# Optimization experiments

Hardware: AMD Instinct MI355X
Metric: run time of the kernel (lower is better)

## Reference

```python
import jax, jax.numpy as jnp
import numpy as np

B, T, N, DIN, HID, ED, K = 64, 12, 1024, 2, 64, 10, 2

def setup_inputs() -> dict:
    key = jax.random.key(0)
    ks = jax.random.split(key, 18)
    g = lambda i, shape, s=0.1: jax.random.normal(ks[i], shape, jnp.float32) * s
    return dict(
        x=g(0, (B, T, N, DIN), 1.0),
        node_embeddings=g(1, (N, ED), 1.0),
        # GCRN cell 0 (dim_in=DIN): gate -> 2*HID, update -> HID
        Wg0=g(2, (ED, K, DIN + HID, 2 * HID)), bg0=g(3, (ED, 2 * HID)),
        Wu0=g(4, (ED, K, DIN + HID, HID)),     bu0=g(5, (ED, HID)),
        # GCRN cell 1 (dim_in=HID)
        Wg1=g(6, (ED, K, 2 * HID, 2 * HID)),   bg1=g(7, (ED, 2 * HID)),
        Wu1=g(8, (ED, K, 2 * HID, HID)),       bu1=g(9, (ED, HID)),
        # RelatinoShipConv: pointwise Linear(input_dim -> rnn_units), torch [out,in]
        Wr=g(10, (HID, DIN)), br=g(11, (HID,)),
        # end_conv1: Linear(HID,HID, bias=False) (num_layers>1 branch)
        W1=g(12, (HID, HID)),
        # self.conv: Conv2d(horizon, horizon, (1, HID+1), bias=False), OIHW
        Wc=g(13, (T, T, 1, HID + 1)),
        # end_conv2: Conv2d(horizon, horizon, (1, HID), bias)
        W2=g(14, (T, T, 1, HID)), b2=g(15, (T,)),
        # end_conv3: Conv2d(horizon, horizon, (1, 2), dilation (1, HID), bias)
        W3=g(16, (T, T, 1, 2)), b3=g(17, (T,)),
    )

def _avwgcn(x, supports, E, Wp, bp):
    # x:[B,N,C], supports:[K,N,N], E:[N,ED] -> [B,N,O]  (AGCRN adaptive graph conv)
    xg = jnp.einsum('knm,bmc->bnkc', supports, x)
    W = jnp.einsum('ne,ekio->nkio', E, Wp)
    b = E @ bp
    return jnp.einsum('bnki,nkio->bno', xg, W) + b

def _cell(xt, h, supports, E, Wg, bg, Wu, bu):
    # GCRN GRU cell
    zr = jax.nn.sigmoid(_avwgcn(jnp.concatenate([xt, h], -1), supports, E, Wg, bg))
    z, r = jnp.split(zr, 2, -1)
    hc = jnp.tanh(_avwgcn(jnp.concatenate([xt, z * h], -1), supports, E, Wu, bu))
    return r * h + (1.0 - r) * hc

def _conv2d(x, w, b=None, rhs_dilation=(1, 1)):
    y = jax.lax.conv_general_dilated(x, w, (1, 1), 'VALID',
        rhs_dilation=rhs_dilation, dimension_numbers=('NCHW', 'OIHW', 'NCHW'))
    return y if b is None else y + b[None, :, None, None]

def _forward(x, E, Wg0, bg0, Wu0, bu0, Wg1, bg1, Wu1, bu1, Wr, br, W1, Wc, W2, b2, W3, b3):
    A = jax.nn.softmax(jax.nn.relu(E @ E.T), axis=1)
    supports = jnp.stack([jnp.eye(N, dtype=x.dtype), A], 0)  # [K,N,N]
    # GCRN encoder: python loop over 2 layers, lax.scan over the 12 timesteps
    cur = x
    for (Wg, bg, Wu, bu) in ((Wg0, bg0, Wu0, bu0), (Wg1, bg1, Wu1, bu1)):
        h0 = jnp.zeros((x.shape[0], N, HID), x.dtype)
        def step(h, xt):
            h = _cell(xt, h, supports, E, Wg, bg, Wu, bu)
            return h, h
        _, hs = jax.lax.scan(step, h0, jnp.swapaxes(cur, 0, 1))
        cur = jnp.swapaxes(hs, 0, 1)  # [B,T,N,HID]
    out = cur @ W1.T  # end_conv1 (Linear, no bias); dropout is identity in eval
    relation = x @ Wr.T + br  # [B,T,N,HID]
    # torch einsum 'btnc,knn->kbcnt' takes the DIAGONAL of supports over n
    rg = jnp.einsum('btnc,knn->kbcnt', relation, supports)
    rg = jnp.transpose(rg, (1, 4, 3, 2, 0)).reshape(x.shape[0], T, N, -1)  # [B,12,N,2*HID]
    rst = _conv2d(rg, Wc)  # [B,12,N,HID]
    out = _conv2d(jnp.concatenate([rst, out], -1), W2, b2)  # [B,12,N,HID+1]
    out = _conv2d(out, W3, b3, rhs_dilation=(1, HID))       # [B,12,N,1]
    return out

def reference(x, node_embeddings, Wg0, bg0, Wu0, bu0, Wg1, bg1, Wu1, bu1, Wr, br, W1, Wc, W2, b2, W3, b3):
    return _forward(x, node_embeddings, Wg0, bg0, Wu0, bu0, Wg1, bg1, Wu1, bu1, Wr, br, W1, Wc, W2, b2, W3, b3)
```

## Files before the change

### kernel.cpp

```cpp
#include <hip/hip_runtime.h>

typedef unsigned short u16;
typedef unsigned int   u32;

__device__ __forceinline__ float bf2f(u16 u){ return __uint_as_float(((u32)u)<<16); }
__device__ __forceinline__ u16 f2bf(float f){
  u32 u = __float_as_uint(f);
  return (u16)((u + 0x7fffu + ((u>>16)&1u)) >> 16);
}

__global__ __launch_bounds__(256) void k_A2(const float* __restrict__ E,
    float* __restrict__ A, float* __restrict__ At, float* __restrict__ diagA)
{
  __shared__ float EL[10][1024];
  __shared__ float row[1024];
  __shared__ float red[4];
  int n = blockIdx.x, tid = threadIdx.x;
  for (int idx=tid; idx<10240; idx+=256)
    EL[idx>>10][idx&1023] = E[(idx&1023)*10 + (idx>>10)];
  __syncthreads();
  float en[10];
#pragma unroll
  for (int e=0;e<10;++e) en[e] = EL[e][n];
  float lmax = -1e30f;
#pragma unroll
  for (int j=0;j<4;++j){
    int m = tid*4 + j;
    float d = 0.f;
#pragma unroll
    for (int e=0;e<10;++e) d = fmaf(en[e], EL[e][m], d);
    d = fmaxf(d, 0.f);
    row[m] = d; lmax = fmaxf(lmax, d);
  }
#pragma unroll
  for (int o=32;o>0;o>>=1) lmax = fmaxf(lmax, __shfl_xor(lmax, o));
  if ((tid&63)==0) red[tid>>6] = lmax;
  __syncthreads();
  float mx = fmaxf(fmaxf(red[0],red[1]), fmaxf(red[2],red[3]));
  __syncthreads();
  float lsum = 0.f;
#pragma unroll
  for (int j=0;j<4;++j){
    int m = tid*4 + j;
    float ex = expf(row[m] - mx);
    row[m] = ex; lsum += ex;
  }
#pragma unroll
  for (int o=32;o>0;o>>=1) lsum += __shfl_xor(lsum, o);
  if ((tid&63)==0) red[tid>>6] = lsum;
  __syncthreads();
  float inv = 1.f/(red[0]+red[1]+red[2]+red[3]);
#pragma unroll
  for (int j=0;j<4;++j){
    int m = tid*4 + j;
    float v = row[m]*inv;
    A[(size_t)n*1024 + m]  = v;
    At[(size_t)m*1024 + n] = v;
    if (m == n) diagA[n] = v;
  }
}

__global__ __launch_bounds__(64) void k_b3eff(
    const float* __restrict__ b2, const float* __restrict__ W3,
    const float* __restrict__ b3, float* __restrict__ b3eff)
{
  int o = threadIdx.x;
  if (o < 12){
    float a = b3[o];
    for (int i=0;i<12;++i)
      a += b2[i] * (W3[(o*12+i)*2] + W3[(o*12+i)*2+1]);
    b3eff[o] = a;
  }
}

__global__ __launch_bounds__(256) void k_Vpre(const float* __restrict__ W1,
    const float* __restrict__ W2, float* __restrict__ V)
{
  int idx = blockIdx.x*256 + threadIdx.x;
  if (idx >= 9216) return;
  int c = idx & 63, r = idx >> 6;
  int j = r % 12, i = r / 12;
  float a = 0.f;
  for (int o=0;o<64;++o)
    a = fmaf(W2[(i*12+j)*64+o], W1[o*64+c], a);
  V[idx] = a;
}

__global__ __launch_bounds__(256) void k_Gpre(const float* __restrict__ Wc,
    const float* __restrict__ W2, u16* __restrict__ G)
{
  int idx = blockIdx.x*256 + threadIdx.x;
  int u = idx & 127, r = idx >> 7;
  int ip = r % 12, i = r / 12;
  float a = 0.f;
  int wlo = u>64 ? u-64 : 0;
  int whi = u<63 ? u : 63;
  for (int j=0;j<12;++j){
    const float* w2r = W2 + (i*12+j)*64;
    const float* wcr = Wc + (j*12+ip)*65;
    for (int w=wlo; w<=whi; ++w)
      a = fmaf(w2r[w], wcr[u-w], a);
  }
  G[idx] = f2bf(a);
}

__global__ __launch_bounds__(256) void gemm4(const float* __restrict__ At,
    const float* __restrict__ X0, float* __restrict__ Y0,
    const float* __restrict__ X1, float* __restrict__ Y1)
{
  const float* X = blockIdx.z ? X1 : X0;
  float*       Y = blockIdx.z ? Y1 : Y0;
  int n0 = blockIdx.x * 128;
  long base = (long)blockIdx.y * 65536;
  __shared__ float Al[32*128];
  __shared__ float Xl[32*64];
  int tid = threadIdx.x;
  int tx = tid & 15, ty = tid >> 4;
  float acc[8][4];
#pragma unroll
  for (int r=0;r<8;++r){ acc[r][0]=0;acc[r][1]=0;acc[r][2]=0;acc[r][3]=0; }

  for (int m0=0; m0<1024; m0+=32){
#pragma unroll
    for (int i=0;i<4;++i){
      int fo = tid + i*256;
      int k = fo >> 5, nl4 = fo & 31;
      float4 v = *(const float4*)(At + (size_t)(m0+k)*1024 + n0 + nl4*4);
      *(float4*)(Al + fo*4) = v;
    }
#pragma unroll
    for (int i=0;i<2;++i){
      int fo = tid + i*256;
      float4 v = *(const float4*)(X + base + (long)m0*64 + fo*4);
      *(float4*)(Xl + fo*4) = v;
    }
    __syncthreads();
#pragma unroll
    for (int kk=0;kk<32;++kk){
      float4 xv = *(const float4*)(Xl + kk*64 + tx*4);
      float4 a0 = *(const float4*)(Al + kk*128 + ty*4);
      float4 a1 = *(const float4*)(Al + kk*128 + 64 + ty*4);
      float av[8] = {a0.x,a0.y,a0.z,a0.w,a1.x,a1.y,a1.z,a1.w};
      float xw[4] = {xv.x,xv.y,xv.z,xv.w};
#pragma unroll
      for (int r=0;r<8;++r)
#pragma unroll
        for (int c=0;c<4;++c) acc[r][c] = fmaf(av[r], xw[c], acc[r][c]);
    }
    __syncthreads();
  }
#pragma unroll
  for (int half=0; half<2; ++half)
#pragma unroll
    for (int i=0;i<4;++i){
      int row = n0 + half*64 + ty*4 + i;
      float4 v; v.x=acc[half*4+i][0]; v.y=acc[half*4+i][1];
      v.z=acc[half*4+i][2]; v.w=acc[half*4+i][3];
      *(float4*)&Y[base + (long)row*64 + tx*4] = v;
    }
}

__global__ __launch_bounds__(256) void gemm2x(const float* __restrict__ A,
    const float* __restrict__ x, float* __restrict__ Y)
{
  __shared__ float As[64][65];
  __shared__ float Xs[64][65];
  int n0 = blockIdx.x*64;
  int q0 = blockIdx.y*64;
  int tid = threadIdx.x, c = tid & 63, rq = tid >> 6;
  float acc[16];
#pragma unroll
  for (int j=0;j<16;++j) acc[j]=0.f;
  for (int m0=0; m0<1024; m0+=64){
#pragma unroll
    for (int j=0;j<16;++j){
      int idx = tid + j*256;
      int r = idx>>6, k = idx&63;
      As[r][k] = A[(size_t)(n0+r)*1024 + m0 + k];
      int qg = q0 + k;
      Xs[r][k] = x[(size_t)(qg>>1)*2048 + (size_t)(m0+r)*2 + (qg&1)];
    }
    __syncthreads();
    for (int k=0;k<64;++k){
      float xv = Xs[k][c];
#pragma unroll
      for (int j=0;j<16;++j) acc[j] = fmaf(As[rq+4*j][k], xv, acc[j]);
    }
    __syncthreads();
  }
#pragma unroll
  for (int j=0;j<16;++j)
    Y[(size_t)(n0+rq+4*j)*1536 + q0 + c] = acc[j];
}

template<int L>
__global__ __launch_bounds__(256) void k_gate2(
    const float* __restrict__ Wg, const float* __restrict__ bgp,
    const float* __restrict__ E,
    const float* __restrict__ xsrc, const float* __restrict__ Axt,
    const float* __restrict__ h, const float* __restrict__ Ah,
    float* __restrict__ zh, float* __restrict__ rb, int t, int first)
{
  constexpr int IX  = (L==0)?2:64;
  constexpr int KI  = 2*(IX+64);
  constexpr int CH  = (L==0)?44:32;
  constexpr int NCH = KI/CH;
  constexpr int O   = 128;
  __shared__ float inp[32][KI];
  __shared__ float Wl[CH][O];
  __shared__ float En[10];
  int n = blockIdx.x, b0 = blockIdx.y*32, tid = threadIdx.x;

  if (tid < 10) En[tid] = E[n*10 + tid];
  for (int idx=tid; idx<32*IX; idx+=256){
    int bl = idx/IX, i = idx - bl*IX; int b = b0+bl;
    inp[bl][i] = (L==0)
      ? xsrc[(size_t)((b*12+t)*1024+n)*2 + i]
      : xsrc[((size_t)b<<16) + (size_t)n*64 + i];
  }
  for (int idx=tid; idx<2048; idx+=256){
    int bl = idx>>6, c = idx&63; int b = b0+bl;
    inp[bl][IX+c] = first ? 0.f : h[((size_t)b<<16) + (size_t)n*64 + c];
  }
  for (int idx=tid; idx<32*IX; idx+=256){
    int bl = idx/IX, i = idx - bl*IX; int b = b0+bl;
    inp[bl][IX+64+i] = (L==0)
      ? Axt[(size_t)n*1536 + (size_t)(b*12+t)*2 + i]
      : Axt[((size_t)b<<16) + (size_t)n*64 + i];
  }
  for (int idx=tid; idx<2048; idx+=256){
    int bl = idx>>6, c = idx&63; int b = b0+bl;
    inp[bl][2*IX+64+c] = first ? 0.f : Ah[((size_t)b<<16) + (size_t)n*64 + c];
  }
  __syncthreads();

  int bg = tid >> 5;
  int og = tid & 31;
  float acc[4][4];
#pragma unroll
  for (int d=0;d<4;++d){
    int o = og*4+d;
    float a = 0.f;
#pragma unroll
    for (int e=0;e<10;++e) a = fmaf(En[e], bgp[e*O+o], a);
#pragma unroll
    for (int bl=0;bl<4;++bl) acc[bl][d] = a;
  }

  for (int ch=0; ch<NCH; ++ch){
    for (int idx=tid; idx<CH*O; idx+=256){
      int i = idx>>7, o = idx&127;
      float a = 0.f;
#pragma unroll
      for (int e=0;e<10;++e)
        a = fmaf(En[e], Wg[((size_t)e*KI + ch*CH + i)*O + o], a);
      Wl[i][o] = a;
    }
    __syncthreads();
    for (int i=0; i<CH; i+=4){
      float4 xq[4], wq[4];
#pragma unroll
      for (int bl=0;bl<4;++bl) xq[bl] = *(const float4*)&inp[bg*4+bl][ch*CH+i];
#pragma unroll
      for (int ii=0;ii<4;++ii) wq[ii] = *(const float4*)&Wl[i+ii][og*4];
      float xv[4][4], wv[4][4];
#pragma unroll
      for (int bl=0;bl<4;++bl){ xv[bl][0]=xq[bl].x; xv[bl][1]=xq[bl].y; xv[bl][2]=xq[bl].z; xv[bl][3]=xq[bl].w; }
#pragma unroll
      for (int ii=0;ii<4;++ii){ wv[ii][0]=wq[ii].x; wv[ii][1]=wq[ii].y; wv[ii][2]=wq[ii].z; wv[ii][3]=wq[ii].w; }
#pragma unroll
      for (int bl=0;bl<4;++bl)
#pragma unroll
        for (int d=0;d<4;++d)
#pragma unroll
          for (int ii=0;ii<4;++ii)
            acc[bl][d] = fmaf(xv[bl][ii], wv[ii][d], acc[bl][d]);
    }
    __syncthreads();
  }

#pragma unroll
  for (int bl=0;bl<4;++bl){
    int b = b0 + bg*4 + bl;
    size_t base = ((size_t)b<<16) + (size_t)n*64;
#pragma unroll
    for (int d=0;d<4;++d){
      int o = og*4 + d;
      float s = 1.f/(1.f+__expf(-acc[bl][d]));
      if (o < 64){
        if (!first) zh[base+o] = s * h[base+o];
      } else {
        rb[base+o-64] = s;
      }
    }
  }
}

template<int L>
__global__ __launch_bounds__(256) void k_upd2(
    const float* __restrict__ Wu, const float* __restrict__ bup,
    const float* __restrict__ E,
    const float* __restrict__ xsrc, const float* __restrict__ Axt,
    const float* __restrict__ zh, const float* __restrict__ Azh,
    const float* __restrict__ rb, float* __restrict__ h, int t, int first)
{
  constexpr int IX  = (L==0)?2:64;
  constexpr int KI  = 2*(IX+64);
  constexpr int CH  = (L==0)?44:64;
  constexpr int NCH = KI/CH;
  constexpr int O   = 64;
  __shared__ float inp[32][KI];
  __shared__ float Wl[CH][O];
  __shared__ float En[10];
  int n = blockIdx.x, b0 = blockIdx.y*32, tid = threadIdx.x;

  if (tid < 10) En[tid] = E[n*10 + tid];
  for (int idx=tid; idx<32*IX; idx+=256){
    int bl = idx/IX, i = idx - bl*IX; int b = b0+bl;
    inp[bl][i] = (L==0)
      ? xsrc[(size_t)((b*12+t)*1024+n)*2 + i]
      : xsrc[((size_t)b<<16) + (size_t)n*64 + i];
  }
  for (int idx=tid; idx<2048; idx+=256){
    int bl = idx>>6, c = idx&63; int b = b0+bl;
    inp[bl][IX+c] = first ? 0.f : zh[((size_t)b<<16) + (size_t)n*64 + c];
  }
  for (int idx=tid; idx<32*IX; idx+=256){
    int bl = idx/IX, i = idx - bl*IX; int b = b0+bl;
    inp[bl][IX+64+i] = (L==0)
      ? Axt[(size_t)n*1536 + (size_t)(b*12+t)*2 + i]
      : Axt[((size_t)b<<16) + (size_t)n*64 + i];
  }
  for (int idx=tid; idx<2048; idx+=256){
    int bl = idx>>6, c = idx&63; int b = b0+bl;
    inp[bl][2*IX+64+c] = first ? 0.f : Azh[((size_t)b<<16) + (size_t)n*64 + c];
  }
  __syncthreads();

  int bg = tid >> 5;
  int og = tid & 31;
  float acc[4][2];
#pragma unroll
  for (int d=0;d<2;++d){
    int o = og*2+d;
    float a = 0.f;
#pragma unroll
    for (int e=0;e<10;++e) a = fmaf(En[e], bup[e*O+o], a);
#pragma unroll
    for (int bl=0;bl<4;++bl) acc[bl][d] = a;
  }

  for (int ch=0; ch<NCH; ++ch){
    for (int idx=tid; idx<CH*O; idx+=256){
      int i = idx>>6, o = idx&63;
      float a = 0.f;
#pragma unroll
      for (int e=0;e<10;++e)
        a = fmaf(En[e], Wu[((size_t)e*KI + ch*CH + i)*O + o], a);
      Wl[i][o] = a;
    }
    __syncthreads();
    for (int i=0; i<CH; i+=4){
      float4 xq[4]; float2 wq[4];
#pragma unroll
      for (int bl=0;bl<4;++bl) xq[bl] = *(const float4*)&inp[bg*4+bl][ch*CH+i];
#pragma unroll
      for (int ii=0;ii<4;++ii) wq[ii] = *(const float2*)&Wl[i+ii][og*2];
      float xv[4][4], wv[4][2];
#pragma unroll
      for (int bl=0;bl<4;++bl){ xv[bl][0]=xq[bl].x; xv[bl][1]=xq[bl].y; xv[bl][2]=xq[bl].z; xv[bl][3]=xq[bl].w; }
#pragma unroll
      for (int ii=0;ii<4;++ii){ wv[ii][0]=wq[ii].x; wv[ii][1]=wq[ii].y; }
#pragma unroll
      for (int bl=0;bl<4;++bl)
#pragma unroll
        for (int d=0;d<2;++d)
#pragma unroll
          for (int ii=0;ii<4;++ii)
            acc[bl][d] = fmaf(xv[bl][ii], wv[ii][d], acc[bl][d]);
    }
    __syncthreads();
  }

#pragma unroll
  for (int bl=0;bl<4;++bl){
    int b = b0 + bg*4 + bl;
    size_t base = ((size_t)b<<16) + (size_t)n*64;
#pragma unroll
    for (int d=0;d<2;++d){
      int o = og*2 + d;
      float hc = tanhf(acc[bl][d]);
      float r  = rb[base+o];
      float h0v = first ? 0.f : h[base+o];
      h[base+o] = r*h0v + (1.f-r)*hc;
    }
  }
}

__global__ __launch_bounds__(256) void k_q1t(const float* __restrict__ h1,
    const float* __restrict__ V, float* __restrict__ q1acc, int t, int first)
{
  __shared__ float VL[12][64];
  int n = blockIdx.x, tid = threadIdx.x;
  for (int idx=tid; idx<768; idx+=256){
    int i = idx>>6, c = idx&63;
    VL[i][c] = V[(i*12+t)*64 + c];
  }
  __syncthreads();
  for (int task=tid; task<768; task+=256){
    int b = task/12, i = task - (task/12)*12;
    const float* hv = h1 + ((size_t)b<<16) + (size_t)n*64;
    float s = 0.f;
#pragma unroll
    for (int c=0;c<64;++c) s = fmaf(hv[c], VL[i][c], s);
    size_t qi = (((size_t)b<<10) + n)*12 + i;
    if (first) q1acc[qi] = s; else q1acc[qi] += s;
  }
}

__global__ __launch_bounds__(256) void k_q0G(
    const float* __restrict__ x, const float* __restrict__ diagA,
    const u16* __restrict__ G,
    const float* __restrict__ Wr, const float* __restrict__ br,
    float* __restrict__ q0buf)
{
  int n = blockIdx.x, tid = threadIdx.x;
  __shared__ u16  GL[18432];
  __shared__ float xsL[64][25];
  __shared__ float WrL[64][2];
  __shared__ float brL[64];

  for (int idx=tid; idx<18432; idx+=256) GL[idx] = G[idx];
  for (int idx=tid; idx<1536; idx+=256){
    int b = idx/24, r = idx - b*24;
    xsL[b][r] = x[(size_t)((b*12+(r>>1))*1024+n)*2 + (r&1)];
  }
  if (tid<128) WrL[tid>>1][tid&1] = Wr[tid];
  else if (tid<192) brL[tid-128] = br[tid-128];
  __syncthreads();

  float dA = diagA[n];
  int b = tid & 63, iq = tid >> 6;
  int i0 = iq*3;
  float q0a=0.f, q0b=0.f, q0c=0.f;
  for (int ip=0; ip<12; ++ip){
    float xa = xsL[b][ip*2], xb = xsL[b][ip*2+1];
    const u16* g0r = &GL[((i0+0)*12+ip)*128];
    const u16* g1r = &GL[((i0+1)*12+ip)*128];
    const u16* g2r = &GL[((i0+2)*12+ip)*128];
    for (int c=0;c<64;++c){
      float rel  = fmaf(xa, WrL[c][0], fmaf(xb, WrL[c][1], brL[c]));
      float relD = rel * dA;
      u32 g0 = *(const u32*)&g0r[2*c];
      u32 g1 = *(const u32*)&g1r[2*c];
      u32 g2 = *(const u32*)&g2r[2*c];
      q0a = fmaf(rel, bf2f((u16)g0), fmaf(relD, bf2f((u16)(g0>>16)), q0a));
      q0b = fmaf(rel, bf2f((u16)g1), fmaf(relD, bf2f((u16)(g1>>16)), q0b));
      q0c = fmaf(rel, bf2f((u16)g2), fmaf(relD, bf2f((u16)(g2>>16)), q0c));
    }
  }
  size_t qb = (((size_t)b<<10) + n)*12;
  q0buf[qb+i0]   = q0a;
  q0buf[qb+i0+1] = q0b;
  q0buf[qb+i0+2] = q0c;
}

__global__ __launch_bounds__(256) void k_head2(
    const float* __restrict__ q0buf, const float* __restrict__ q1acc,
    const float* __restrict__ W3, const float* __restrict__ b3eff,
    float* __restrict__ out)
{
  int n = blockIdx.x, tid = threadIdx.x;
  __shared__ float W3L[12][12][2];
  __shared__ float b3eL[12];
  __shared__ float q0L[64][12];
  __shared__ float q1L[64][12];

  if (tid < 12) b3eL[tid] = b3eff[tid];
  for (int idx=tid; idx<288; idx+=256){
    int o = idx/24, r = idx - o*24;
    W3L[o][r>>1][r&1] = W3[idx];
  }
  for (int idx=tid; idx<768; idx+=256){
    int b = idx/12, i = idx - (idx/12)*12;
    size_t base = (((size_t)b<<10) + n)*12 + i;
    q0L[b][i] = q0buf[base];
    q1L[b][i] = q1acc[base];
  }
  __syncthreads();

  for (int idx=tid; idx<768; idx+=256){
    int bb = idx/12, o = idx - (idx/12)*12;
    float a = b3eL[o];
#pragma unroll
    for (int i=0;i<12;++i)
      a += q0L[bb][i]*W3L[o][i][0] + q1L[bb][i]*W3L[o][i][1];
    out[(size_t)(bb*12+o)*1024 + n] = a;
  }
}

extern "C" void kernel_launch(void* const* d_in, const int* in_sizes, int n_in,
                              void* d_out, int out_size, void* d_ws, size_t ws_size,
                              hipStream_t stream)
{
  const float* x   = (const float*)d_in[0];
  const float* E   = (const float*)d_in[1];
  const float* Wg0 = (const float*)d_in[2];
  const float* bg0 = (const float*)d_in[3];
  const float* Wu0 = (const float*)d_in[4];
  const float* bu0 = (const float*)d_in[5];
  const float* Wg1 = (const float*)d_in[6];
  const float* bg1 = (const float*)d_in[7];
  const float* Wu1 = (const float*)d_in[8];
  const float* bu1 = (const float*)d_in[9];
  const float* Wr  = (const float*)d_in[10];
  const float* br  = (const float*)d_in[11];
  const float* W1  = (const float*)d_in[12];
  const float* Wc  = (const float*)d_in[13];
  const float* W2  = (const float*)d_in[14];
  const float* b2  = (const float*)d_in[15];
  const float* W3  = (const float*)d_in[16];
  const float* b3  = (const float*)d_in[17];

  char* ws = (char*)d_ws;
  size_t off = 0;
  auto alloc = [&](size_t bytes)->void*{
    void* p = ws + off; off += (bytes + 255) & ~(size_t)255; return p;
  };
  float* A     = (float*)alloc(1024ull*1024*4);
  float* At    = (float*)alloc(1024ull*1024*4);
  float* diagA = (float*)alloc(1024*4);
  float* Ax0T  = (float*)alloc(1024ull*1536*4);
  float* AhZ0  = (float*)alloc(64ull*65536*4);
  float* AhZ1  = (float*)alloc(64ull*65536*4);
  float* zh    = (float*)alloc(64ull*65536*4);
  float* rb    = (float*)alloc(64ull*65536*4);
  float* Axt1  = (float*)alloc(64ull*65536*4);
  float* h0    = (float*)alloc(64ull*65536*4);
  float* h1    = (float*)alloc(64ull*65536*4);
  float* q1acc = (float*)alloc(64ull*1024*12*4);
  float* q0buf = (float*)alloc(64ull*1024*12*4);
  float* V     = (float*)alloc(12ull*12*64*4);
  u16*   G     = (u16*)alloc(12ull*12*128*2);
  float* b3eff = (float*)alloc(12*4);

  if (off > ws_size) return;

  k_A2<<<dim3(1024),256,0,stream>>>(E, A, At, diagA);
  k_b3eff<<<dim3(1),64,0,stream>>>(b2, W3, b3, b3eff);
  k_Vpre<<<dim3(36),256,0,stream>>>(W1, W2, V);
  k_Gpre<<<dim3(72),256,0,stream>>>(Wc, W2, G);
  gemm2x<<<dim3(16,24),256,0,stream>>>(A, x, Ax0T);
  k_q0G<<<dim3(1024),256,0,stream>>>(x, diagA, G, Wr, br, q0buf);

  for (int t=0;t<12;++t){
    int first = (t==0);
    k_gate2<0><<<dim3(1024,2),256,0,stream>>>(Wg0, bg0, E, x, Ax0T, h0, Axt1,
                                              zh, rb, t, first);
    if (!first) gemm4<<<dim3(8,64,1),256,0,stream>>>(At, zh, AhZ0, nullptr, nullptr);
    k_upd2<0><<<dim3(1024,2),256,0,stream>>>(Wu0, bu0, E, x, Ax0T, zh, AhZ0,
                                             rb, h0, t, first);
    gemm4<<<dim3(8,64, first?1:2),256,0,stream>>>(At, h0, Axt1, h1, AhZ1);
    k_gate2<1><<<dim3(1024,2),256,0,stream>>>(Wg1, bg1, E, h0, Axt1, h1, AhZ1,
                                              zh, rb, t, first);
    if (!first) gemm4<<<dim3(8,64,1),256,0,stream>>>(At, zh, AhZ0, nullptr, nullptr);
    k_upd2<1><<<dim3(1024,2),256,0,stream>>>(Wu1, bu1, E, h0, Axt1, zh, AhZ0,
                                             rb, h1, t, first);
    k_q1t<<<dim3(1024),256,0,stream>>>(h1, V, q1acc, t, first);
  }

  k_head2<<<dim3(1024),256,0,stream>>>(q0buf, q1acc, W3, b3eff, (float*)d_out);
}
```

Baseline: 10.48 ms.

## Double-buffer the adjacency GEMM, prefetch operands in gate/update loops, fuse q1 projection

The adjacency GEMM now double-buffers its shared-memory tiles. It loads the next global tile into registers while computing the current one and prefetches the LDS operands one k-step ahead. The gate and update kernels software-pipeline their shared-memory operand reads in the same way. The per-timestep q1 projection kernel is folded into the layer-1 update kernel, which reuses the Wl shared buffer to hold the new hidden state and V, removing a launch and a re-read of h1. These changes raise register and LDS use, which may lower occupancy.

```diff
diff --git a/kernel.cpp b/kernel.cpp
--- a/kernel.cpp
+++ b/kernel.cpp
@@ -104,7 +104,7 @@
   G[idx] = f2bf(a);
 }
 
-__global__ __launch_bounds__(256) void gemm4(const float* __restrict__ At,
+__global__ __launch_bounds__(256) void gemm5(const float* __restrict__ At,
     const float* __restrict__ X0, float* __restrict__ Y0,
     const float* __restrict__ X1, float* __restrict__ Y1)
 {
@@ -112,40 +112,73 @@
   float*       Y = blockIdx.z ? Y1 : Y0;
   int n0 = blockIdx.x * 128;
   long base = (long)blockIdx.y * 65536;
-  __shared__ float Al[32*128];
-  __shared__ float Xl[32*64];
+  __shared__ float Al[2][4096];
+  __shared__ float Xl[2][2048];
   int tid = threadIdx.x;
   int tx = tid & 15, ty = tid >> 4;
+
+  float4 ra0, ra1, ra2, ra3, rx0, rx1;
+  int ka[4], na[4];
+#pragma unroll
+  for (int i=0;i<4;++i){
+    int fo = tid + i*256;
+    ka[i] = fo >> 5; na[i] = (fo & 31)*4;
+  }
+
   float acc[8][4];
 #pragma unroll
   for (int r=0;r<8;++r){ acc[r][0]=0;acc[r][1]=0;acc[r][2]=0;acc[r][3]=0; }
 
+  ra0 = *(const float4*)(At + (size_t)(ka[0])*1024 + n0 + na[0]);
+  ra1 = *(const float4*)(At + (size_t)(ka[1])*1024 + n0 + na[1]);
+  ra2 = *(const float4*)(At + (size_t)(ka[2])*1024 + n0 + na[2]);
+  ra3 = *(const float4*)(At + (size_t)(ka[3])*1024 + n0 + na[3]);
+  rx0 = *(const float4*)(X + base + (long)(tid      )*4);
+  rx1 = *(const float4*)(X + base + (long)(tid + 256)*4);
+  *(float4*)(Al[0] + (tid      )*4) = ra0;
+  *(float4*)(Al[0] + (tid+ 256 )*4) = ra1;
+  *(float4*)(Al[0] + (tid+ 512 )*4) = ra2;
+  *(float4*)(Al[0] + (tid+ 768 )*4) = ra3;
+  *(float4*)(Xl[0] + (tid      )*4) = rx0;
+  *(float4*)(Xl[0] + (tid+ 256 )*4) = rx1;
+  __syncthreads();
+
   for (int m0=0; m0<1024; m0+=32){
-#pragma unroll
-    for (int i=0;i<4;++i){
-      int fo = tid + i*256;
-      int k = fo >> 5, nl4 = fo & 31;
-      float4 v = *(const float4*)(At + (size_t)(m0+k)*1024 + n0 + nl4*4);
-      *(float4*)(Al + fo*4) = v;
-    }
-#pragma unroll
-    for (int i=0;i<2;++i){
-      int fo = tid + i*256;
-      float4 v = *(const float4*)(X + base + (long)m0*64 + fo*4);
-      *(float4*)(Xl + fo*4) = v;
-    }
-    __syncthreads();
-#pragma unroll
-    for (int kk=0;kk<32;++kk){
-      float4 xv = *(const float4*)(Xl + kk*64 + tx*4);
-      float4 a0 = *(const float4*)(Al + kk*128 + ty*4);
-      float4 a1 = *(const float4*)(Al + kk*128 + 64 + ty*4);
+    int cur = (m0>>5)&1, nxt = cur^1;
+    bool more = (m0+32 < 1024);
+    if (more){
+      int m1 = m0 + 32;
+      ra0 = *(const float4*)(At + (size_t)(m1+ka[0])*1024 + n0 + na[0]);
+      ra1 = *(const float4*)(At + (size_t)(m1+ka[1])*1024 + n0 + na[1]);
+      ra2 = *(const float4*)(At + (size_t)(m1+ka[2])*1024 + n0 + na[2]);
+      ra3 = *(const float4*)(At + (size_t)(m1+ka[3])*1024 + n0 + na[3]);
+      rx0 = *(const float4*)(X + base + (long)m1*64 + (long)(tid      )*4);
+      rx1 = *(const float4*)(X + base + (long)m1*64 + (long)(tid + 256)*4);
+    }
+    float4 xv = *(const float4*)(Xl[cur] + tx*4);
+    float4 a0 = *(const float4*)(Al[cur] + ty*4);
+    float4 a1 = *(const float4*)(Al[cur] + 64 + ty*4);
+#pragma unroll
+    for (int kk=0; kk<32; ++kk){
+      int k1 = (kk<31) ? kk+1 : kk;
+      float4 xn  = *(const float4*)(Xl[cur] + k1*64 + tx*4);
+      float4 an0 = *(const float4*)(Al[cur] + k1*128 + ty*4);
+      float4 an1 = *(const float4*)(Al[cur] + k1*128 + 64 + ty*4);
       float av[8] = {a0.x,a0.y,a0.z,a0.w,a1.x,a1.y,a1.z,a1.w};
       float xw[4] = {xv.x,xv.y,xv.z,xv.w};
 #pragma unroll
       for (int r=0;r<8;++r)
 #pragma unroll
         for (int c=0;c<4;++c) acc[r][c] = fmaf(av[r], xw[c], acc[r][c]);
+      xv=xn; a0=an0; a1=an1;
+    }
+    if (more){
+      *(float4*)(Al[nxt] + (tid      )*4) = ra0;
+      *(float4*)(Al[nxt] + (tid+ 256 )*4) = ra1;
+      *(float4*)(Al[nxt] + (tid+ 512 )*4) = ra2;
+      *(float4*)(Al[nxt] + (tid+ 768 )*4) = ra3;
+      *(float4*)(Xl[nxt] + (tid      )*4) = rx0;
+      *(float4*)(Xl[nxt] + (tid+ 256 )*4) = rx1;
     }
     __syncthreads();
   }
@@ -257,12 +290,18 @@
       Wl[i][o] = a;
     }
     __syncthreads();
+    float4 xq[4], wq[4];
+#pragma unroll
+    for (int bl=0;bl<4;++bl) xq[bl] = *(const float4*)&inp[bg*4+bl][ch*CH];
+#pragma unroll
+    for (int ii=0;ii<4;++ii) wq[ii] = *(const float4*)&Wl[ii][og*4];
     for (int i=0; i<CH; i+=4){
-      float4 xq[4], wq[4];
-#pragma unroll
-      for (int bl=0;bl<4;++bl) xq[bl] = *(const float4*)&inp[bg*4+bl][ch*CH+i];
-#pragma unroll
-      for (int ii=0;ii<4;++ii) wq[ii] = *(const float4*)&Wl[i+ii][og*4];
+      int i2 = (i+4<CH) ? i+4 : i;
+      float4 xq2[4], wq2[4];
+#pragma unroll
+      for (int bl=0;bl<4;++bl) xq2[bl] = *(const float4*)&inp[bg*4+bl][ch*CH+i2];
+#pragma unroll
+      for (int ii=0;ii<4;++ii) wq2[ii] = *(const float4*)&Wl[i2+ii][og*4];
       float xv[4][4], wv[4][4];
 #pragma unroll
       for (int bl=0;bl<4;++bl){ xv[bl][0]=xq[bl].x; xv[bl][1]=xq[bl].y; xv[bl][2]=xq[bl].z; xv[bl][3]=xq[bl].w; }
@@ -275,6 +314,10 @@
 #pragma unroll
           for (int ii=0;ii<4;++ii)
             acc[bl][d] = fmaf(xv[bl][ii], wv[ii][d], acc[bl][d]);
+#pragma unroll
+      for (int bl=0;bl<4;++bl) xq[bl]=xq2[bl];
+#pragma unroll
+      for (int ii=0;ii<4;++ii) wq[ii]=wq2[ii];
     }
     __syncthreads();
   }
@@ -302,7 +345,9 @@
     const float* __restrict__ E,
     const float* __restrict__ xsrc, const float* __restrict__ Axt,
     const float* __restrict__ zh, const float* __restrict__ Azh,
-    const float* __restrict__ rb, float* __restrict__ h, int t, int first)
+    const float* __restrict__ rb, float* __restrict__ h,
+    const float* __restrict__ V, float* __restrict__ q1acc,
+    int t, int first)
 {
   constexpr int IX  = (L==0)?2:64;
   constexpr int KI  = 2*(IX+64);
@@ -360,12 +405,18 @@
       Wl[i][o] = a;
     }
     __syncthreads();
+    float4 xq[4]; float2 wq[4];
+#pragma unroll
+    for (int bl=0;bl<4;++bl) xq[bl] = *(const float4*)&inp[bg*4+bl][ch*CH];
+#pragma unroll
+    for (int ii=0;ii<4;++ii) wq[ii] = *(const float2*)&Wl[ii][og*2];
     for (int i=0; i<CH; i+=4){
-      float4 xq[4]; float2 wq[4];
-#pragma unroll
-      for (int bl=0;bl<4;++bl) xq[bl] = *(const float4*)&inp[bg*4+bl][ch*CH+i];
-#pragma unroll
-      for (int ii=0;ii<4;++ii) wq[ii] = *(const float2*)&Wl[i+ii][og*2];
+      int i2 = (i+4<CH) ? i+4 : i;
+      float4 xq2[4]; float2 wq2[4];
+#pragma unroll
+      for (int bl=0;bl<4;++bl) xq2[bl] = *(const float4*)&inp[bg*4+bl][ch*CH+i2];
+#pragma unroll
+      for (int ii=0;ii<4;++ii) wq2[ii] = *(const float2*)&Wl[i2+ii][og*2];
       float xv[4][4], wv[4][2];
 #pragma unroll
       for (int bl=0;bl<4;++bl){ xv[bl][0]=xq[bl].x; xv[bl][1]=xq[bl].y; xv[bl][2]=xq[bl].z; xv[bl][3]=xq[bl].w; }
@@ -378,10 +429,16 @@
 #pragma unroll
           for (int ii=0;ii<4;++ii)
             acc[bl][d] = fmaf(xv[bl][ii], wv[ii][d], acc[bl][d]);
-    }
-    __syncthreads();
-  }
-
+#pragma unroll
+      for (int bl=0;bl<4;++bl) xq[bl]=xq2[bl];
+#pragma unroll
+      for (int ii=0;ii<4;++ii) wq[ii]=wq2[ii];
+    }
+    __syncthreads();
+  }
+
+  float* hnL = (float*)Wl;
+  float* VL  = ((float*)Wl) + 2080;
 #pragma unroll
   for (int bl=0;bl<4;++bl){
     int b = b0 + bg*4 + bl;
@@ -392,29 +449,25 @@
       float hc = tanhf(acc[bl][d]);
       float r  = rb[base+o];
       float h0v = first ? 0.f : h[base+o];
-      h[base+o] = r*h0v + (1.f-r)*hc;
-    }
-  }
-}
-
-__global__ __launch_bounds__(256) void k_q1t(const float* __restrict__ h1,
-    const float* __restrict__ V, float* __restrict__ q1acc, int t, int first)
-{
-  __shared__ float VL[12][64];
-  int n = blockIdx.x, tid = threadIdx.x;
-  for (int idx=tid; idx<768; idx+=256){
-    int i = idx>>6, c = idx&63;
-    VL[i][c] = V[(i*12+t)*64 + c];
-  }
-  __syncthreads();
-  for (int task=tid; task<768; task+=256){
-    int b = task/12, i = task - (task/12)*12;
-    const float* hv = h1 + ((size_t)b<<16) + (size_t)n*64;
-    float s = 0.f;
-#pragma unroll
-    for (int c=0;c<64;++c) s = fmaf(hv[c], VL[i][c], s);
-    size_t qi = (((size_t)b<<10) + n)*12 + i;
-    if (first) q1acc[qi] = s; else q1acc[qi] += s;
+      float hn = r*h0v + (1.f-r)*hc;
+      h[base+o] = hn;
+      if (L==1) hnL[(bg*4+bl)*65 + o] = hn;
+    }
+  }
+  if (L==1){
+    for (int idx=tid; idx<768; idx+=256)
+      VL[idx] = V[((idx>>6)*12+t)*64 + (idx&63)];
+    __syncthreads();
+    for (int task=tid; task<384; task+=256){
+      int bl = task & 31, i = task >> 5;
+      const float* hv = hnL + bl*65;
+      const float* vv = VL + i*64;
+      float s = 0.f;
+#pragma unroll 8
+      for (int c=0;c<64;++c) s = fmaf(hv[c], vv[c], s);
+      size_t qi = (((size_t)(b0+bl)<<10) + n)*12 + i;
+      if (first) q1acc[qi] = s; else q1acc[qi] += s;
+    }
   }
 }
 
@@ -557,16 +610,15 @@
     int first = (t==0);
     k_gate2<0><<<dim3(1024,2),256,0,stream>>>(Wg0, bg0, E, x, Ax0T, h0, Axt1,
                                               zh, rb, t, first);
-    if (!first) gemm4<<<dim3(8,64,1),256,0,stream>>>(At, zh, AhZ0, nullptr, nullptr);
+    if (!first) gemm5<<<dim3(8,64,1),256,0,stream>>>(At, zh, AhZ0, nullptr, nullptr);
     k_upd2<0><<<dim3(1024,2),256,0,stream>>>(Wu0, bu0, E, x, Ax0T, zh, AhZ0,
-                                             rb, h0, t, first);
-    gemm4<<<dim3(8,64, first?1:2),256,0,stream>>>(At, h0, Axt1, h1, AhZ1);
+                                             rb, h0, nullptr, nullptr, t, first);
+    gemm5<<<dim3(8,64, first?1:2),256,0,stream>>>(At, h0, Axt1, h1, AhZ1);
     k_gate2<1><<<dim3(1024,2),256,0,stream>>>(Wg1, bg1, E, h0, Axt1, h1, AhZ1,
                                               zh, rb, t, first);
-    if (!first) gemm4<<<dim3(8,64,1),256,0,stream>>>(At, zh, AhZ0, nullptr, nullptr);
+    if (!first) gemm5<<<dim3(8,64,1),256,0,stream>>>(At, zh, AhZ0, nullptr, nullptr);
     k_upd2<1><<<dim3(1024,2),256,0,stream>>>(Wu1, bu1, E, h0, Axt1, zh, AhZ0,
-                                             rb, h1, t, first);
-    k_q1t<<<dim3(1024),256,0,stream>>>(h1, V, q1acc, t, first);
+                                             rb, h1, V, q1acc, t, first);
   }
 
   k_head2<<<dim3(1024),256,0,stream>>>(q0buf, q1acc, W3, b3eff, (float*)d_out);
```

Result: slower. 12.64 ms (+20.7%).

## Wavefront-schedule the two GRU layers, batching layer-0 step t+1 with layer-1 step t

Applied to the files above, without the earlier changes.

Restructures the recurrence as a wavefront: each iteration runs layer-1 at step k and layer-0 at step k+1 in the same launches, using blockIdx.z to select the layer, with double-buffered h0 and separate zh/rb/Azh buffers per layer. It also fuses the q1 projection into the layer-1 update kernel and register-prefetches the next shared-memory operands in the gate and update inner loops. The aim is fewer launches per timestep and bigger grids that fill the GPU better, at the cost of more workspace and more complex buffer indexing.

```diff
diff --git a/kernel.cpp b/kernel.cpp
--- a/kernel.cpp
+++ b/kernel.cpp
@@ -2,6 +2,7 @@
 
 typedef unsigned short u16;
 typedef unsigned int   u32;
+
 
 __device__ __forceinline__ float bf2f(u16 u){ return __uint_as_float(((u32)u)<<16); }
 __device__ __forceinline__ u16 f2bf(float f){
@@ -104,7 +105,7 @@
   G[idx] = f2bf(a);
 }
 
-__global__ __launch_bounds__(256) void gemm4(const float* __restrict__ At,
+__global__ __launch_bounds__(256) void gemm7(const float* __restrict__ At,
     const float* __restrict__ X0, float* __restrict__ Y0,
     const float* __restrict__ X1, float* __restrict__ Y1)
 {
@@ -194,43 +195,41 @@
 }
 
 template<int L>
-__global__ __launch_bounds__(256) void k_gate2(
+__device__ __forceinline__ void gate_body(
+    float* __restrict__ inp, float* __restrict__ Wl, float* __restrict__ En,
     const float* __restrict__ Wg, const float* __restrict__ bgp,
     const float* __restrict__ E,
     const float* __restrict__ xsrc, const float* __restrict__ Axt,
     const float* __restrict__ h, const float* __restrict__ Ah,
-    float* __restrict__ zh, float* __restrict__ rb, int t, int first)
+    float* __restrict__ zh, float* __restrict__ rb, int t, int first,
+    int n, int b0, int tid)
 {
   constexpr int IX  = (L==0)?2:64;
   constexpr int KI  = 2*(IX+64);
   constexpr int CH  = (L==0)?44:32;
   constexpr int NCH = KI/CH;
   constexpr int O   = 128;
-  __shared__ float inp[32][KI];
-  __shared__ float Wl[CH][O];
-  __shared__ float En[10];
-  int n = blockIdx.x, b0 = blockIdx.y*32, tid = threadIdx.x;
 
   if (tid < 10) En[tid] = E[n*10 + tid];
   for (int idx=tid; idx<32*IX; idx+=256){
     int bl = idx/IX, i = idx - bl*IX; int b = b0+bl;
-    inp[bl][i] = (L==0)
+    inp[bl*KI + i] = (L==0)
       ? xsrc[(size_t)((b*12+t)*1024+n)*2 + i]
       : xsrc[((size_t)b<<16) + (size_t)n*64 + i];
   }
   for (int idx=tid; idx<2048; idx+=256){
     int bl = idx>>6, c = idx&63; int b = b0+bl;
-    inp[bl][IX+c] = first ? 0.f : h[((size_t)b<<16) + (size_t)n*64 + c];
+    inp[bl*KI + IX + c] = first ? 0.f : h[((size_t)b<<16) + (size_t)n*64 + c];
   }
   for (int idx=tid; idx<32*IX; idx+=256){
     int bl = idx/IX, i = idx - bl*IX; int b = b0+bl;
-    inp[bl][IX+64+i] = (L==0)
+    inp[bl*KI + IX+64+i] = (L==0)
       ? Axt[(size_t)n*1536 + (size_t)(b*12+t)*2 + i]
       : Axt[((size_t)b<<16) + (size_t)n*64 + i];
   }
   for (int idx=tid; idx<2048; idx+=256){
     int bl = idx>>6, c = idx&63; int b = b0+bl;
-    inp[bl][2*IX+64+c] = first ? 0.f : Ah[((size_t)b<<16) + (size_t)n*64 + c];
+    inp[bl*KI + 2*IX+64+c] = first ? 0.f : Ah[((size_t)b<<16) + (size_t)n*64 + c];
   }
   __syncthreads();
 
@@ -254,15 +253,21 @@
 #pragma unroll
       for (int e=0;e<10;++e)
         a = fmaf(En[e], Wg[((size_t)e*KI + ch*CH + i)*O + o], a);
-      Wl[i][o] = a;
-    }
-    __syncthreads();
+      Wl[i*O + o] = a;
+    }
+    __syncthreads();
+    float4 xq[4], wq[4];
+#pragma unroll
+    for (int bl=0;bl<4;++bl) xq[bl] = *(const float4*)&inp[(bg*4+bl)*KI + ch*CH];
+#pragma unroll
+    for (int ii=0;ii<4;++ii) wq[ii] = *(const float4*)&Wl[ii*O + og*4];
     for (int i=0; i<CH; i+=4){
-      float4 xq[4], wq[4];
-#pragma unroll
-      for (int bl=0;bl<4;++bl) xq[bl] = *(const float4*)&inp[bg*4+bl][ch*CH+i];
-#pragma unroll
-      for (int ii=0;ii<4;++ii) wq[ii] = *(const float4*)&Wl[i+ii][og*4];
+      int i2 = (i+4<CH) ? i+4 : i;
+      float4 xq2[4], wq2[4];
+#pragma unroll
+      for (int bl=0;bl<4;++bl) xq2[bl] = *(const float4*)&inp[(bg*4+bl)*KI + ch*CH + i2];
+#pragma unroll
+      for (int ii=0;ii<4;++ii) wq2[ii] = *(const float4*)&Wl[(i2+ii)*O + og*4];
       float xv[4][4], wv[4][4];
 #pragma unroll
       for (int bl=0;bl<4;++bl){ xv[bl][0]=xq[bl].x; xv[bl][1]=xq[bl].y; xv[bl][2]=xq[bl].z; xv[bl][3]=xq[bl].w; }
@@ -275,6 +280,10 @@
 #pragma unroll
           for (int ii=0;ii<4;++ii)
             acc[bl][d] = fmaf(xv[bl][ii], wv[ii][d], acc[bl][d]);
+#pragma unroll
+      for (int bl=0;bl<4;++bl) xq[bl]=xq2[bl];
+#pragma unroll
+      for (int ii=0;ii<4;++ii) wq[ii]=wq2[ii];
     }
     __syncthreads();
   }
@@ -296,44 +305,67 @@
   }
 }
 
+__global__ __launch_bounds__(256) void k_gateB(int l_z0,
+    const float* __restrict__ Wg0, const float* __restrict__ bg0,
+    const float* __restrict__ Wg1, const float* __restrict__ bg1,
+    const float* __restrict__ E,  const float* __restrict__ x,
+    const float* __restrict__ Ax0T,
+    const float* __restrict__ h0cur, const float* __restrict__ h1,
+    const float* __restrict__ Axt1,  const float* __restrict__ AhZ1,
+    float* __restrict__ zh0, float* __restrict__ rb0,
+    float* __restrict__ zh1, float* __restrict__ rb1,
+    int t0, int first0, int first1)
+{
+  __shared__ float smem[12288];
+  __shared__ float En[10];
+  int n = blockIdx.x, b0 = blockIdx.y*32, tid = threadIdx.x;
+  int L = blockIdx.z ? 0 : l_z0;
+  if (L == 1)
+    gate_body<1>(smem, smem + 32*256, En, Wg1, bg1, E,
+                 h0cur, Axt1, h1, AhZ1, zh1, rb1, 0, first1, n, b0, tid);
+  else
+    gate_body<0>(smem, smem + 32*132, En, Wg0, bg0, E,
+                 x, Ax0T, h0cur, Axt1, zh0, rb0, t0, first0, n, b0, tid);
+}
+
 template<int L>
-__global__ __launch_bounds__(256) void k_upd2(
+__device__ __forceinline__ void upd_body(
+    float* __restrict__ inp, float* __restrict__ Wl, float* __restrict__ En,
     const float* __restrict__ Wu, const float* __restrict__ bup,
     const float* __restrict__ E,
     const float* __restrict__ xsrc, const float* __restrict__ Axt,
     const float* __restrict__ zh, const float* __restrict__ Azh,
-    const float* __restrict__ rb, float* __restrict__ h, int t, int first)
+    const float* __restrict__ rb,
+    const float* __restrict__ hread, float* __restrict__ hwrite,
+    const float* __restrict__ V, float* __restrict__ q1acc,
+    int t, int tq, int first, int n, int b0, int tid)
 {
   constexpr int IX  = (L==0)?2:64;
   constexpr int KI  = 2*(IX+64);
   constexpr int CH  = (L==0)?44:64;
   constexpr int NCH = KI/CH;
   constexpr int O   = 64;
-  __shared__ float inp[32][KI];
-  __shared__ float Wl[CH][O];
-  __shared__ float En[10];
-  int n = blockIdx.x, b0 = blockIdx.y*32, tid = threadIdx.x;
 
   if (tid < 10) En[tid] = E[n*10 + tid];
   for (int idx=tid; idx<32*IX; idx+=256){
     int bl = idx/IX, i = idx - bl*IX; int b = b0+bl;
-    inp[bl][i] = (L==0)
+    inp[bl*KI + i] = (L==0)
       ? xsrc[(size_t)((b*12+t)*1024+n)*2 + i]
       : xsrc[((size_t)b<<16) + (size_t)n*64 + i];
   }
   for (int idx=tid; idx<2048; idx+=256){
     int bl = idx>>6, c = idx&63; int b = b0+bl;
-    inp[bl][IX+c] = first ? 0.f : zh[((size_t)b<<16) + (size_t)n*64 + c];
+    inp[bl*KI + IX + c] = first ? 0.f : zh[((size_t)b<<16) + (size_t)n*64 + c];
   }
   for (int idx=tid; idx<32*IX; idx+=256){
     int bl = idx/IX, i = idx - bl*IX; int b = b0+bl;
-    inp[bl][IX+64+i] = (L==0)
+    inp[bl*KI + IX+64+i] = (L==0)
       ? Axt[(size_t)n*1536 + (size_t)(b*12+t)*2 + i]
       : Axt[((size_t)b<<16) + (size_t)n*64 + i];
   }
   for (int idx=tid; idx<2048; idx+=256){
     int bl = idx>>6, c = idx&63; int b = b0+bl;
-    inp[bl][2*IX+64+c] = first ? 0.f : Azh[((size_t)b<<16) + (size_t)n*64 + c];
+    inp[bl*KI + 2*IX+64+c] = first ? 0.f : Azh[((size_t)b<<16) + (size_t)n*64 + c];
   }
   __syncthreads();
 
@@ -357,15 +389,21 @@
 #pragma unroll
       for (int e=0;e<10;++e)
         a = fmaf(En[e], Wu[((size_t)e*KI + ch*CH + i)*O + o], a);
-      Wl[i][o] = a;
-    }
-    __syncthreads();
+      Wl[i*O + o] = a;
+    }
+    __syncthreads();
+    float4 xq[4]; float2 wq[4];
+#pragma unroll
+    for (int bl=0;bl<4;++bl) xq[bl] = *(const float4*)&inp[(bg*4+bl)*KI + ch*CH];
+#pragma unroll
+    for (int ii=0;ii<4;++ii) wq[ii] = *(const float2*)&Wl[ii*O + og*2];
     for (int i=0; i<CH; i+=4){
-      float4 xq[4]; float2 wq[4];
-#pragma unroll
-      for (int bl=0;bl<4;++bl) xq[bl] = *(const float4*)&inp[bg*4+bl][ch*CH+i];
-#pragma unroll
-      for (int ii=0;ii<4;++ii) wq[ii] = *(const float2*)&Wl[i+ii][og*2];
+      int i2 = (i+4<CH) ? i+4 : i;
+      float4 xq2[4]; float2 wq2[4];
+#pragma unroll
+      for (int bl=0;bl<4;++bl) xq2[bl] = *(const float4*)&inp[(bg*4+bl)*KI + ch*CH + i2];
+#pragma unroll
+      for (int ii=0;ii<4;++ii) wq2[ii] = *(const float2*)&Wl[(i2+ii)*O + og*2];
       float xv[4][4], wv[4][2];
 #pragma unroll
       for (int bl=0;bl<4;++bl){ xv[bl][0]=xq[bl].x; xv[bl][1]=xq[bl].y; xv[bl][2]=xq[bl].z; xv[bl][3]=xq[bl].w; }
@@ -378,10 +416,16 @@
 #pragma unroll
           for (int ii=0;ii<4;++ii)
             acc[bl][d] = fmaf(xv[bl][ii], wv[ii][d], acc[bl][d]);
-    }
-    __syncthreads();
-  }
-
+#pragma unroll
+      for (int bl=0;bl<4;++bl) xq[bl]=xq2[bl];
+#pragma unroll
+      for (int ii=0;ii<4;++ii) wq[ii]=wq2[ii];
+    }
+    __syncthreads();
+  }
+
+  float* hnL = Wl;
+  float* VL  = Wl + 2080;
 #pragma unroll
   for (int bl=0;bl<4;++bl){
     int b = b0 + bg*4 + bl;
@@ -391,31 +435,55 @@
       int o = og*2 + d;
       float hc = tanhf(acc[bl][d]);
       float r  = rb[base+o];
-      float h0v = first ? 0.f : h[base+o];
-      h[base+o] = r*h0v + (1.f-r)*hc;
-    }
-  }
-}
-
-__global__ __launch_bounds__(256) void k_q1t(const float* __restrict__ h1,
-    const float* __restrict__ V, float* __restrict__ q1acc, int t, int first)
-{
-  __shared__ float VL[12][64];
-  int n = blockIdx.x, tid = threadIdx.x;
-  for (int idx=tid; idx<768; idx+=256){
-    int i = idx>>6, c = idx&63;
-    VL[i][c] = V[(i*12+t)*64 + c];
-  }
-  __syncthreads();
-  for (int task=tid; task<768; task+=256){
-    int b = task/12, i = task - (task/12)*12;
-    const float* hv = h1 + ((size_t)b<<16) + (size_t)n*64;
-    float s = 0.f;
-#pragma unroll
-    for (int c=0;c<64;++c) s = fmaf(hv[c], VL[i][c], s);
-    size_t qi = (((size_t)b<<10) + n)*12 + i;
-    if (first) q1acc[qi] = s; else q1acc[qi] += s;
-  }
+      float h0v = first ? 0.f : hread[base+o];
+      float hn = r*h0v + (1.f-r)*hc;
+      hwrite[base+o] = hn;
+      if (L==1) hnL[(bg*4+bl)*65 + o] = hn;
+    }
+  }
+  if (L==1){
+    for (int idx=tid; idx<768; idx+=256)
+      VL[idx] = V[((idx>>6)*12+tq)*64 + (idx&63)];
+    __syncthreads();
+    for (int task=tid; task<384; task+=256){
+      int bl = task & 31, i = task >> 5;
+      const float* hv = hnL + bl*65;
+      const float* vv = VL + i*64;
+      float s = 0.f;
+#pragma unroll 8
+      for (int c=0;c<64;++c) s = fmaf(hv[c], vv[c], s);
+      size_t qi = (((size_t)(b0+bl)<<10) + n)*12 + i;
+      if (first) q1acc[qi] = s; else q1acc[qi] += s;
+    }
+  }
+}
+
+__global__ __launch_bounds__(256) void k_updB(int l_z0,
+    const float* __restrict__ Wu0, const float* __restrict__ bu0,
+    const float* __restrict__ Wu1, const float* __restrict__ bu1,
+    const float* __restrict__ E,  const float* __restrict__ x,
+    const float* __restrict__ Ax0T, const float* __restrict__ Axt1,
+    const float* __restrict__ h0cur, float* __restrict__ h0new,
+    float* __restrict__ h1,
+    const float* __restrict__ zh0, const float* __restrict__ Azh0,
+    const float* __restrict__ rb0,
+    const float* __restrict__ zh1, const float* __restrict__ Azh1,
+    const float* __restrict__ rb1,
+    const float* __restrict__ V, float* __restrict__ q1acc,
+    int t0, int t1, int first0, int first1)
+{
+  __shared__ float smem[12288];
+  __shared__ float En[10];
+  int n = blockIdx.x, b0 = blockIdx.y*32, tid = threadIdx.x;
+  int L = blockIdx.z ? 0 : l_z0;
+  if (L == 1)
+    upd_body<1>(smem, smem + 32*256, En, Wu1, bu1, E,
+                h0cur, Axt1, zh1, Azh1, rb1, h1, h1, V, q1acc,
+                0, t1, first1, n, b0, tid);
+  else
+    upd_body<0>(smem, smem + 32*132, En, Wu0, bu0, E,
+                x, Ax0T, zh0, Azh0, rb0, h0cur, h0new, nullptr, nullptr,
+                t0, 0, first0, n, b0, tid);
 }
 
 __global__ __launch_bounds__(256) void k_q0G(
@@ -531,12 +599,16 @@
   float* At    = (float*)alloc(1024ull*1024*4);
   float* diagA = (float*)alloc(1024*4);
   float* Ax0T  = (float*)alloc(1024ull*1536*4);
-  float* AhZ0  = (float*)alloc(64ull*65536*4);
+  float* Axt1  = (float*)alloc(64ull*65536*4);
   float* AhZ1  = (float*)alloc(64ull*65536*4);
-  float* zh    = (float*)alloc(64ull*65536*4);
-  float* rb    = (float*)alloc(64ull*65536*4);
-  float* Axt1  = (float*)alloc(64ull*65536*4);
-  float* h0    = (float*)alloc(64ull*65536*4);
+  float* Azh0  = (float*)alloc(64ull*65536*4);
+  float* Azh1  = (float*)alloc(64ull*65536*4);
+  float* zh0   = (float*)alloc(64ull*65536*4);
+  float* zh1   = (float*)alloc(64ull*65536*4);
+  float* rb0   = (float*)alloc(64ull*65536*4);
+  float* rb1   = (float*)alloc(64ull*65536*4);
+  float* h0a   = (float*)alloc(64ull*65536*4);
+  float* h0b   = (float*)alloc(64ull*65536*4);
   float* h1    = (float*)alloc(64ull*65536*4);
   float* q1acc = (float*)alloc(64ull*1024*12*4);
   float* q0buf = (float*)alloc(64ull*1024*12*4);
@@ -553,20 +625,35 @@
   gemm2x<<<dim3(16,24),256,0,stream>>>(A, x, Ax0T);
   k_q0G<<<dim3(1024),256,0,stream>>>(x, diagA, G, Wr, br, q0buf);
 
-  for (int t=0;t<12;++t){
-    int first = (t==0);
-    k_gate2<0><<<dim3(1024,2),256,0,stream>>>(Wg0, bg0, E, x, Ax0T, h0, Axt1,
-                                              zh, rb, t, first);
-    if (!first) gemm4<<<dim3(8,64,1),256,0,stream>>>(At, zh, AhZ0, nullptr, nullptr);
-    k_upd2<0><<<dim3(1024,2),256,0,stream>>>(Wu0, bu0, E, x, Ax0T, zh, AhZ0,
-                                             rb, h0, t, first);
-    gemm4<<<dim3(8,64, first?1:2),256,0,stream>>>(At, h0, Axt1, h1, AhZ1);
-    k_gate2<1><<<dim3(1024,2),256,0,stream>>>(Wg1, bg1, E, h0, Axt1, h1, AhZ1,
-                                              zh, rb, t, first);
-    if (!first) gemm4<<<dim3(8,64,1),256,0,stream>>>(At, zh, AhZ0, nullptr, nullptr);
-    k_upd2<1><<<dim3(1024,2),256,0,stream>>>(Wu1, bu1, E, h0, Axt1, zh, AhZ0,
-                                             rb, h1, t, first);
-    k_q1t<<<dim3(1024),256,0,stream>>>(h1, V, q1acc, t, first);
+  k_gateB<<<dim3(1024,2,1),256,0,stream>>>(0, Wg0,bg0, Wg1,bg1, E, x, Ax0T,
+      h0a, h1, Axt1, AhZ1, zh0, rb0, zh1, rb1, 0, 1, 0);
+  k_updB<<<dim3(1024,2,1),256,0,stream>>>(0, Wu0,bu0, Wu1,bu1, E, x, Ax0T, Axt1,
+      h0a, h0a, h1, zh0, Azh0, rb0, zh1, Azh1, rb1, V, q1acc, 0, 0, 1, 0);
+  gemm7<<<dim3(8,64,1),256,0,stream>>>(At, h0a, Axt1, nullptr, nullptr);
+
+  for (int k=0; k<12; ++k){
+    int last   = (k == 11);
+    int first1 = (k == 0);
+    float* h0cur = (k&1) ? h0b : h0a;
+    float* h0new = (k&1) ? h0a : h0b;
+
+    k_gateB<<<dim3(1024,2, last?1:2),256,0,stream>>>(1, Wg0,bg0, Wg1,bg1,
+        E, x, Ax0T, h0cur, h1, Axt1, AhZ1,
+        zh0, rb0, zh1, rb1, k+1, 0, first1);
+
+    if (first1)
+      gemm7<<<dim3(8,64,1),256,0,stream>>>(At, zh0, Azh0, nullptr, nullptr);
+    else if (last)
+      gemm7<<<dim3(8,64,1),256,0,stream>>>(At, zh1, Azh1, nullptr, nullptr);
+    else
+      gemm7<<<dim3(8,64,2),256,0,stream>>>(At, zh1, Azh1, zh0, Azh0);
+
+    k_updB<<<dim3(1024,2, last?1:2),256,0,stream>>>(1, Wu0,bu0, Wu1,bu1,
+        E, x, Ax0T, Axt1, h0cur, h0new, h1,
+        zh0, Azh0, rb0, zh1, Azh1, rb1, V, q1acc, k+1, k, 0, first1);
+
+    if (!last)
+      gemm7<<<dim3(8,64,2),256,0,stream>>>(At, h1, AhZ1, h0new, Axt1);
   }
 
   k_head2<<<dim3(1024),256,0,stream>>>(q0buf, q1acc, W3, b3eff, (float*)d_out);
```

New measurement: 10.36 ms. No clear change (-1.2%).
